# Performance work log

Measured on AMD Instinct MI355X. Metric: run time of the kernel, lower is better.

## Reference

```python
import jax, jax.numpy as jnp
import numpy as np

H = 1024          # h_dim
FF = 4 * H
E = 8             # num_expert
TOP_K = 2


def setup_inputs() -> dict:
    key = jax.random.key(0)
    ks = jax.random.split(key, 7)
    B, S = 4, 2048
    s = 0.02
    return {
        "x": jax.random.normal(ks[0], (B, S, H), dtype=jnp.float32),
        "Wg": jax.random.normal(ks[1], (H, E), dtype=jnp.float32) * s,
        "bg": jnp.zeros((E,), dtype=jnp.float32),
        "W1": jax.random.normal(ks[2], (E, H, FF), dtype=jnp.float32) * s,
        "b1": jnp.zeros((E, FF), dtype=jnp.float32),
        "W2": jax.random.normal(ks[3], (E, FF, H), dtype=jnp.float32) * s,
        "b2": jnp.zeros((E, H), dtype=jnp.float32),
    }


def _moe(x, Wg, bg, W1, b1, W2, b2):
    B, S, h = x.shape
    hs = x.reshape(-1, h)                                  # [T, H]
    logits = hs @ Wg + bg                                  # [T, E]
    probs = jax.nn.softmax(logits.astype(jnp.float32), axis=-1)
    w, idx = jax.lax.top_k(probs, TOP_K)                   # [T, K]
    w = jax.nn.softmax(w, axis=-1).astype(x.dtype)         # renormalize over top-k
    out = jnp.zeros_like(hs)
    for e in range(E):
        # per-token combine weight for expert e (0 if not selected)
        w_e = jnp.sum(w * (idx == e), axis=-1)             # [T]
        y = jax.nn.relu(hs @ W1[e] + b1[e]) @ W2[e] + b2[e]  # [T, H]
        out = out + w_e[:, None] * y
    return out.reshape(B, S, h), logits


def reference(x, Wg, bg, W1, b1, W2, b2):
    return _moe(x, Wg, bg, W1, b1, W2, b2)
```

## Files before the change

kernel.cpp:

```cpp
#include <hip/hip_runtime.h>
#include <hip/hip_bf16.h>

#define T_TOKENS 8192
#define HD 1024
#define FF 4096
#define NEXP 8
#define TOPK 2
#define NR_MAX 17408

typedef __attribute__((ext_vector_type(8))) short bf16x8;
typedef __attribute__((ext_vector_type(4))) float f32x4;

static __device__ __forceinline__ float b2f(ushort u) {
    union { unsigned u; float f; } c; c.u = ((unsigned)u) << 16; return c.f;
}
static __device__ __forceinline__ ushort f2b(float f) {
    union { float f; unsigned u; } c; c.f = f;
    unsigned r = c.u + 0x7fffu + ((c.u >> 16) & 1u);
    return (ushort)(r >> 16);
}

__global__ __launch_bounds__(256) void gate_kernel(
    const float* __restrict__ x, const float* __restrict__ Wg, const float* __restrict__ bg,
    float* __restrict__ logits, int* __restrict__ counts,
    int* __restrict__ e0a, int* __restrict__ e1a,
    float* __restrict__ w0a, float* __restrict__ w1a)
{
    int t = blockIdx.x * 4 + (threadIdx.x >> 6);
    int l = threadIdx.x & 63;
    const float* xr = x + (size_t)t * HD;
    float acc[8] = {0,0,0,0,0,0,0,0};
    #pragma unroll
    for (int i = 0; i < 4; ++i) {
        int h0 = i * 256 + l * 4;
        float4 xv = *(const float4*)(xr + h0);
        #pragma unroll
        for (int j = 0; j < 4; ++j) {
            float xs = (&xv.x)[j];
            const float4* wr = (const float4*)(Wg + (size_t)(h0 + j) * NEXP);
            float4 wa = wr[0], wb = wr[1];
            acc[0] = fmaf(xs, wa.x, acc[0]);
            acc[1] = fmaf(xs, wa.y, acc[1]);
            acc[2] = fmaf(xs, wa.z, acc[2]);
            acc[3] = fmaf(xs, wa.w, acc[3]);
            acc[4] = fmaf(xs, wb.x, acc[4]);
            acc[5] = fmaf(xs, wb.y, acc[5]);
            acc[6] = fmaf(xs, wb.z, acc[6]);
            acc[7] = fmaf(xs, wb.w, acc[7]);
        }
    }
    #pragma unroll
    for (int off = 32; off > 0; off >>= 1) {
        #pragma unroll
        for (int e = 0; e < 8; ++e) acc[e] += __shfl_down(acc[e], off, 64);
    }
    if (l == 0) {
        float lg[8];
        #pragma unroll
        for (int e = 0; e < 8; ++e) {
            lg[e] = acc[e] + bg[e];
            logits[(size_t)t * NEXP + e] = lg[e];
        }
        float m = lg[0];
        #pragma unroll
        for (int e = 1; e < 8; ++e) m = fmaxf(m, lg[e]);
        float p[8], s = 0.f;
        #pragma unroll
        for (int e = 0; e < 8; ++e) { p[e] = expf(lg[e] - m); s += p[e]; }
        float inv = 1.f / s;
        #pragma unroll
        for (int e = 0; e < 8; ++e) p[e] *= inv;
        int i0 = 0;
        #pragma unroll
        for (int e = 1; e < 8; ++e) if (p[e] > p[i0]) i0 = e;
        int i1 = (i0 == 0) ? 1 : 0;
        #pragma unroll
        for (int e = 0; e < 8; ++e) if (e != i0 && p[e] > p[i1]) i1 = e;
        float ed = expf(p[i1] - p[i0]);
        float w0 = 1.f / (1.f + ed);
        float w1 = ed / (1.f + ed);
        e0a[t] = i0; e1a[t] = i1; w0a[t] = w0; w1a[t] = w1;
        atomicAdd(&counts[i0], 1);
        atomicAdd(&counts[i1], 1);
    }
}

__global__ void offsets_kernel(const int* __restrict__ counts, int* __restrict__ off) {
    if (threadIdx.x == 0) {
        int o = 0;
        for (int e = 0; e < 8; ++e) { off[e] = o; o += (counts[e] + 127) & ~127; }
        off[8] = o;
    }
}

__global__ __launch_bounds__(256) void assign_kernel(
    const int* __restrict__ e0a, const int* __restrict__ e1a,
    const int* __restrict__ off, int* __restrict__ fill,
    int* __restrict__ row0, int* __restrict__ row1, int* __restrict__ row_token)
{
    int t = blockIdx.x * 256 + threadIdx.x;
    if (t >= T_TOKENS) return;
    int e0 = e0a[t];
    int r0 = off[e0] + atomicAdd(&fill[e0], 1);
    row0[t] = r0; row_token[r0] = t;
    int e1 = e1a[t];
    int r1 = off[e1] + atomicAdd(&fill[e1], 1);
    row1[t] = r1; row_token[r1] = t;
}

__global__ __launch_bounds__(256) void gather_kernel(
    const float* __restrict__ x, const int* __restrict__ row_token, ushort* __restrict__ Xp)
{
    int r = blockIdx.x;
    int tok = row_token[r];
    int c = threadIdx.x * 4;
    ushort4 o;
    if (tok >= 0 && tok < T_TOKENS) {
        float4 v = *(const float4*)(x + (size_t)tok * HD + c);
        o.x = f2b(v.x); o.y = f2b(v.y); o.z = f2b(v.z); o.w = f2b(v.w);
    } else {
        o.x = 0; o.y = 0; o.z = 0; o.w = 0;
    }
    *(ushort4*)(Xp + (size_t)r * HD + c) = o;
}

__global__ __launch_bounds__(256) void transpose_cvt_kernel(
    const float* __restrict__ in, ushort* __restrict__ out, int R, int C)
{
    __shared__ ushort tile[64][65];
    size_t esz = (size_t)R * C;
    const float* ein = in + (size_t)blockIdx.z * esz;
    ushort* eout = out + (size_t)blockIdx.z * esz;
    int c0 = blockIdx.x * 64, r0 = blockIdx.y * 64;
    int tr = threadIdx.x >> 4;
    int tc = (threadIdx.x & 15) * 4;
    #pragma unroll
    for (int i = 0; i < 4; ++i) {
        int r = tr + i * 16;
        float4 v = *(const float4*)(ein + (size_t)(r0 + r) * C + c0 + tc);
        tile[r][tc + 0] = f2b(v.x);
        tile[r][tc + 1] = f2b(v.y);
        tile[r][tc + 2] = f2b(v.z);
        tile[r][tc + 3] = f2b(v.w);
    }
    __syncthreads();
    #pragma unroll
    for (int i = 0; i < 4; ++i) {
        int cc = tr + i * 16;
        ushort4 o;
        o.x = tile[tc + 0][cc];
        o.y = tile[tc + 1][cc];
        o.z = tile[tc + 2][cc];
        o.w = tile[tc + 3][cc];
        *(ushort4*)(eout + (size_t)(c0 + cc) * R + r0 + tc) = o;
    }
}

template<int K, int NTOT, bool RELU>
__global__ __launch_bounds__(256) void gemm_kernel(
    const ushort* __restrict__ A, const ushort* __restrict__ Bt,
    const float* __restrict__ bias, ushort* __restrict__ Out,
    const int* __restrict__ off)
{
    __shared__ __align__(16) ushort lds[2][2][128 * 32];
    int r0 = blockIdx.y * 128;
    int total = off[8];
    if (r0 >= total) return;
    int e = 0;
    #pragma unroll
    for (int q = 0; q < 7; ++q) if (r0 >= off[q + 1]) e = q + 1;

    int tid = threadIdx.x;
    int w = tid >> 6, lane = tid & 63;
    int wr = w >> 1, wc = w & 1;
    int lr = lane & 15, lk = lane >> 4;
    int ntile = blockIdx.x;

    const ushort* Ab = A + (size_t)r0 * K;
    const ushort* Bb = Bt + (size_t)e * NTOT * K + (size_t)ntile * 128 * K;

    auto stage = [&](const ushort* gbase, ushort* ldsbase) {
        #pragma unroll
        for (int issue = 0; issue < 2; ++issue) {
            int row = issue * 64 + w * 16 + (lane >> 2);
            int chunk = (lane & 3) ^ ((lane >> 3) & 3);
            const ushort* g = gbase + (size_t)row * K + chunk * 8;
            ushort* lp = ldsbase + (issue * 64 + w * 16) * 32;
            __builtin_amdgcn_global_load_lds(
                (const __attribute__((address_space(1))) void*)g,
                (__attribute__((address_space(3))) void*)lp, 16, 0, 0);
        }
    };

    stage(Ab, &lds[0][0][0]);
    stage(Bb, &lds[0][1][0]);

    f32x4 acc[4][4];
    #pragma unroll
    for (int mi = 0; mi < 4; ++mi)
        #pragma unroll
        for (int ni = 0; ni < 4; ++ni) acc[mi][ni] = (f32x4){0.f, 0.f, 0.f, 0.f};

    __syncthreads();

    constexpr int KT = K / 32;
    int cur = 0;
    int slot = lk ^ ((lr >> 1) & 3);
    for (int kt = 0; kt < KT; ++kt) {
        if (kt + 1 < KT) {
            stage(Ab + (kt + 1) * 32, &lds[cur ^ 1][0][0]);
            stage(Bb + (kt + 1) * 32, &lds[cur ^ 1][1][0]);
        }
        const ushort* As = &lds[cur][0][0];
        const ushort* Bs = &lds[cur][1][0];
        bf16x8 a[4], b[4];
        #pragma unroll
        for (int mi = 0; mi < 4; ++mi)
            a[mi] = *(const bf16x8*)(As + (wr * 64 + mi * 16 + lr) * 32 + slot * 8);
        #pragma unroll
        for (int ni = 0; ni < 4; ++ni)
            b[ni] = *(const bf16x8*)(Bs + (wc * 64 + ni * 16 + lr) * 32 + slot * 8);
        #pragma unroll
        for (int mi = 0; mi < 4; ++mi)
            #pragma unroll
            for (int ni = 0; ni < 4; ++ni)
                acc[mi][ni] = __builtin_amdgcn_mfma_f32_16x16x32_bf16(
                    a[mi], b[ni], acc[mi][ni], 0, 0, 0);
        __syncthreads();
        cur ^= 1;
    }

    int c0 = ntile * 128 + wc * 64;
    int rbase = r0 + wr * 64;
    #pragma unroll
    for (int ni = 0; ni < 4; ++ni) {
        int n = c0 + ni * 16 + lr;
        float bv = bias[(size_t)e * NTOT + n];
        #pragma unroll
        for (int mi = 0; mi < 4; ++mi) {
            int m = rbase + mi * 16 + lk * 4;
            #pragma unroll
            for (int j = 0; j < 4; ++j) {
                float v = acc[mi][ni][j] + bv;
                if (RELU) v = fmaxf(v, 0.f);
                Out[(size_t)(m + j) * NTOT + n] = f2b(v);
            }
        }
    }
}

__global__ __launch_bounds__(256) void combine_kernel(
    const ushort* __restrict__ Y, const int* __restrict__ row0, const int* __restrict__ row1,
    const float* __restrict__ w0a, const float* __restrict__ w1a, float* __restrict__ out)
{
    int t = blockIdx.x;
    int c = threadIdx.x * 4;
    int r0 = row0[t], r1 = row1[t];
    float w0 = w0a[t], w1 = w1a[t];
    ushort4 ya = *(const ushort4*)(Y + (size_t)r0 * HD + c);
    ushort4 yb = *(const ushort4*)(Y + (size_t)r1 * HD + c);
    float4 o;
    o.x = w0 * b2f(ya.x) + w1 * b2f(yb.x);
    o.y = w0 * b2f(ya.y) + w1 * b2f(yb.y);
    o.z = w0 * b2f(ya.z) + w1 * b2f(yb.z);
    o.w = w0 * b2f(ya.w) + w1 * b2f(yb.w);
    *(float4*)(out + (size_t)t * HD + c) = o;
}

#define WSA(x) (((x) + 255) & ~(size_t)255)
static constexpr size_t OFF_COUNTS = 0;
static constexpr size_t OFF_FILL   = 64;
static constexpr size_t OFF_OFF    = 128;
static constexpr size_t OFF_E0     = 256;
static constexpr size_t OFF_E1     = OFF_E0 + (size_t)T_TOKENS * 4;
static constexpr size_t OFF_W0     = OFF_E1 + (size_t)T_TOKENS * 4;
static constexpr size_t OFF_W1A    = OFF_W0 + (size_t)T_TOKENS * 4;
static constexpr size_t OFF_R0     = OFF_W1A + (size_t)T_TOKENS * 4;
static constexpr size_t OFF_R1     = OFF_R0 + (size_t)T_TOKENS * 4;
static constexpr size_t OFF_RT     = OFF_R1 + (size_t)T_TOKENS * 4;
static constexpr size_t OFF_XP     = WSA(OFF_RT + (size_t)NR_MAX * 4);
static constexpr size_t OFF_W1T    = OFF_XP  + (size_t)NR_MAX * HD * 2;
static constexpr size_t OFF_W2T    = OFF_W1T + (size_t)NEXP * FF * HD * 2;
static constexpr size_t OFF_H1     = OFF_W2T + (size_t)NEXP * HD * FF * 2;
static constexpr size_t OFF_Y      = OFF_H1  + (size_t)NR_MAX * FF * 2;
static constexpr size_t WS_NEEDED  = OFF_Y   + (size_t)NR_MAX * HD * 2;

extern "C" void kernel_launch(void* const* d_in, const int* in_sizes, int n_in,
                              void* d_out, int out_size, void* d_ws, size_t ws_size,
                              hipStream_t stream) {
    (void)in_sizes; (void)n_in; (void)out_size;
    const float* x  = (const float*)d_in[0];
    const float* Wg = (const float*)d_in[1];
    const float* bg = (const float*)d_in[2];
    const float* W1 = (const float*)d_in[3];
    const float* b1 = (const float*)d_in[4];
    const float* W2 = (const float*)d_in[5];
    const float* b2 = (const float*)d_in[6];
    float* out    = (float*)d_out;
    float* logits = out + (size_t)T_TOKENS * HD;

    if (ws_size < WS_NEEDED) return;

    char* ws = (char*)d_ws;
    int*    counts = (int*)(ws + OFF_COUNTS);
    int*    fill   = (int*)(ws + OFF_FILL);
    int*    offp   = (int*)(ws + OFF_OFF);
    int*    e0a    = (int*)(ws + OFF_E0);
    int*    e1a    = (int*)(ws + OFF_E1);
    float*  w0a    = (float*)(ws + OFF_W0);
    float*  w1a    = (float*)(ws + OFF_W1A);
    int*    row0   = (int*)(ws + OFF_R0);
    int*    row1   = (int*)(ws + OFF_R1);
    int*    rowtok = (int*)(ws + OFF_RT);
    ushort* Xp     = (ushort*)(ws + OFF_XP);
    ushort* W1T    = (ushort*)(ws + OFF_W1T);
    ushort* W2T    = (ushort*)(ws + OFF_W2T);
    ushort* H1     = (ushort*)(ws + OFF_H1);
    ushort* Y      = (ushort*)(ws + OFF_Y);

    hipMemsetAsync(ws, 0, 256, stream);
    hipMemsetAsync(rowtok, 0xFF, (size_t)NR_MAX * 4, stream);

    gate_kernel<<<T_TOKENS / 4, 256, 0, stream>>>(x, Wg, bg, logits, counts, e0a, e1a, w0a, w1a);
    offsets_kernel<<<1, 64, 0, stream>>>(counts, offp);
    assign_kernel<<<T_TOKENS / 256, 256, 0, stream>>>(e0a, e1a, offp, fill, row0, row1, rowtok);
    gather_kernel<<<NR_MAX, 256, 0, stream>>>(x, rowtok, Xp);
    transpose_cvt_kernel<<<dim3(FF / 64, HD / 64, NEXP), 256, 0, stream>>>(W1, W1T, HD, FF);
    transpose_cvt_kernel<<<dim3(HD / 64, FF / 64, NEXP), 256, 0, stream>>>(W2, W2T, FF, HD);
    gemm_kernel<HD, FF, true><<<dim3(FF / 128, NR_MAX / 128), 256, 0, stream>>>(Xp, W1T, b1, H1, offp);
    gemm_kernel<FF, HD, false><<<dim3(HD / 128, NR_MAX / 128), 256, 0, stream>>>(H1, W2T, b2, Y, offp);
    combine_kernel<<<T_TOKENS, 256, 0, stream>>>(Y, row0, row1, w0a, w1a, out);
}
```

Baseline: 794.0 us.

## Rewrite expert GEMMs with 256-row tiles, 8 waves, 4-stage LDS pipeline

```diff
diff --git a/kernel.cpp b/kernel.cpp
--- a/kernel.cpp
+++ b/kernel.cpp
@@ -5,8 +5,7 @@
 #define HD 1024
 #define FF 4096
 #define NEXP 8
-#define TOPK 2
-#define NR_MAX 17408
+#define NR_MAX 18432
 
 typedef __attribute__((ext_vector_type(8))) short bf16x8;
 typedef __attribute__((ext_vector_type(4))) float f32x4;
@@ -88,7 +87,7 @@
 __global__ void offsets_kernel(const int* __restrict__ counts, int* __restrict__ off) {
     if (threadIdx.x == 0) {
         int o = 0;
-        for (int e = 0; e < 8; ++e) { off[e] = o; o += (counts[e] + 127) & ~127; }
+        for (int e = 0; e < 8; ++e) { off[e] = o; o += (counts[e] + 255) & ~255; }
         off[8] = o;
     }
 }
@@ -156,14 +155,32 @@
     }
 }
 
-template<int K, int NTOT, bool RELU>
-__global__ __launch_bounds__(256) void gemm_kernel(
+template<int K, int NTOT, bool RELU, int BN, int WM, int WN>
+__global__ __launch_bounds__(512, 2) void gemm8p_kernel(
     const ushort* __restrict__ A, const ushort* __restrict__ Bt,
     const float* __restrict__ bias, ushort* __restrict__ Out,
     const int* __restrict__ off)
 {
-    __shared__ __align__(16) ushort lds[2][2][128 * 32];
-    int r0 = blockIdx.y * 128;
+    constexpr int BM = 256, BK = 32;
+    constexpr int MREP = BM / (WM * 16);
+    constexpr int NREP = BN / (WN * 16);
+    constexpr int PHASES = (MREP * NREP) / 16;
+    constexpr int MPP = MREP / PHASES;
+    constexpr int A_ISS = (BM * BK) / (512 * 8);
+    constexpr int B_ISS = (BN * BK) / (512 * 8);
+    constexpr int LPT = A_ISS + B_ISS;
+    constexpr int KT = K / BK;
+    constexpr int NT = NTOT / BN;
+
+    __shared__ __align__(16) ushort ldsA[4][BM * BK];
+    __shared__ __align__(16) ushort ldsB[4][BN * BK];
+
+    int nwg = gridDim.x;
+    int bid = blockIdx.x;
+    int wgid = (bid & 7) * (nwg >> 3) + (bid >> 3);
+    int ntile = wgid % NT;
+    int mtile = wgid / NT;
+    int r0 = mtile * BM;
     int total = off[8];
     if (r0 >= total) return;
     int e = 0;
@@ -171,73 +188,122 @@
     for (int q = 0; q < 7; ++q) if (r0 >= off[q + 1]) e = q + 1;
 
     int tid = threadIdx.x;
-    int w = tid >> 6, lane = tid & 63;
-    int wr = w >> 1, wc = w & 1;
+    int wid = tid >> 6, lane = tid & 63;
+    int wr = wid / WN, wc = wid % WN;
     int lr = lane & 15, lk = lane >> 4;
-    int ntile = blockIdx.x;
 
     const ushort* Ab = A + (size_t)r0 * K;
-    const ushort* Bb = Bt + (size_t)e * NTOT * K + (size_t)ntile * 128 * K;
-
-    auto stage = [&](const ushort* gbase, ushort* ldsbase) {
-        #pragma unroll
-        for (int issue = 0; issue < 2; ++issue) {
-            int row = issue * 64 + w * 16 + (lane >> 2);
-            int chunk = (lane & 3) ^ ((lane >> 3) & 3);
-            const ushort* g = gbase + (size_t)row * K + chunk * 8;
-            ushort* lp = ldsbase + (issue * 64 + w * 16) * 32;
+    const ushort* Bb = Bt + ((size_t)e * NTOT + (size_t)ntile * BN) * K;
+
+    int srow = tid >> 2;
+    int schunk = (tid & 3) ^ (srow & 3);
+
+    auto stageA = [&](int kt) {
+        ushort* dst = &ldsA[kt & 3][tid * 8];
+        const ushort* g = Ab + (size_t)kt * BK + (size_t)srow * K + schunk * 8;
+        #pragma unroll
+        for (int i = 0; i < A_ISS; ++i)
             __builtin_amdgcn_global_load_lds(
-                (const __attribute__((address_space(1))) void*)g,
-                (__attribute__((address_space(3))) void*)lp, 16, 0, 0);
+                (const __attribute__((address_space(1))) void*)(g + (size_t)i * 128 * K),
+                (__attribute__((address_space(3))) void*)(dst + i * 4096),
+                16, 0, 0);
+    };
+    auto stageB = [&](int kt) {
+        ushort* dst = &ldsB[kt & 3][tid * 8];
+        const ushort* g = Bb + (size_t)kt * BK + (size_t)srow * K + schunk * 8;
+        #pragma unroll
+        for (int i = 0; i < B_ISS; ++i)
+            __builtin_amdgcn_global_load_lds(
+                (const __attribute__((address_space(1))) void*)(g + (size_t)i * 128 * K),
+                (__attribute__((address_space(3))) void*)(dst + i * 4096),
+                16, 0, 0);
+    };
+    auto ldA = [&](int slot, int m) -> bf16x8 {
+        int row = wr * (BM / WM) + m * 16 + lr;
+        int chunk = lk ^ (row & 3);
+        return *(const bf16x8*)&ldsA[slot][row * 32 + chunk * 8];
+    };
+    auto ldB = [&](int slot, int n) -> bf16x8 {
+        int row = wc * (BN / WN) + n * 16 + lr;
+        int chunk = lk ^ (row & 3);
+        return *(const bf16x8*)&ldsB[slot][row * 32 + chunk * 8];
+    };
+
+    f32x4 acc[MREP][NREP];
+    #pragma unroll
+    for (int m = 0; m < MREP; ++m)
+        #pragma unroll
+        for (int n = 0; n < NREP; ++n) acc[m][n] = (f32x4){0.f, 0.f, 0.f, 0.f};
+
+    stageA(0); stageB(0);
+    stageA(1); stageB(1);
+    stageA(2); stageB(2);
+    asm volatile("s_waitcnt vmcnt(%0)" :: "n"(2 * LPT) : "memory");
+    __builtin_amdgcn_sched_barrier(0);
+    __builtin_amdgcn_s_barrier();
+    __builtin_amdgcn_sched_barrier(0);
+
+    for (int kt = 0; kt < KT; ++kt) {
+        int slot = kt & 3;
+        bf16x8 a0[MPP], b[NREP];
+        #pragma unroll
+        for (int m = 0; m < MPP; ++m) a0[m] = ldA(slot, m);
+        #pragma unroll
+        for (int n = 0; n < NREP; ++n) b[n] = ldB(slot, n);
+        if (kt + 3 < KT) { stageA(kt + 3); if (PHASES == 1) stageB(kt + 3); }
+        __builtin_amdgcn_sched_barrier(0);
+        __builtin_amdgcn_s_barrier();
+        asm volatile("s_waitcnt lgkmcnt(0)" ::: "memory");
+        __builtin_amdgcn_sched_barrier(0);
+        __builtin_amdgcn_s_setprio(1);
+        __builtin_amdgcn_sched_barrier(0);
+        #pragma unroll
+        for (int m = 0; m < MPP; ++m)
+            #pragma unroll
+            for (int n = 0; n < NREP; ++n)
+                acc[m][n] = __builtin_amdgcn_mfma_f32_16x16x32_bf16(a0[m], b[n], acc[m][n], 0, 0, 0);
+        __builtin_amdgcn_sched_barrier(0);
+        __builtin_amdgcn_s_setprio(0);
+        __builtin_amdgcn_sched_barrier(0);
+
+        if constexpr (PHASES == 2) {
+            __builtin_amdgcn_s_barrier();
+            bf16x8 a1[MPP];
+            #pragma unroll
+            for (int m = 0; m < MPP; ++m) a1[m] = ldA(slot, MPP + m);
+            if (kt + 3 < KT) stageB(kt + 3);
+            __builtin_amdgcn_sched_barrier(0);
+            __builtin_amdgcn_s_barrier();
+            asm volatile("s_waitcnt lgkmcnt(0)" ::: "memory");
+            __builtin_amdgcn_sched_barrier(0);
+            __builtin_amdgcn_s_setprio(1);
+            __builtin_amdgcn_sched_barrier(0);
+            #pragma unroll
+            for (int m = 0; m < MPP; ++m)
+                #pragma unroll
+                for (int n = 0; n < NREP; ++n)
+                    acc[MPP + m][n] = __builtin_amdgcn_mfma_f32_16x16x32_bf16(a1[m], b[n], acc[MPP + m][n], 0, 0, 0);
+            __builtin_amdgcn_sched_barrier(0);
+            __builtin_amdgcn_s_setprio(0);
+            __builtin_amdgcn_sched_barrier(0);
         }
-    };
-
-    stage(Ab, &lds[0][0][0]);
-    stage(Bb, &lds[0][1][0]);
-
-    f32x4 acc[4][4];
-    #pragma unroll
-    for (int mi = 0; mi < 4; ++mi)
-        #pragma unroll
-        for (int ni = 0; ni < 4; ++ni) acc[mi][ni] = (f32x4){0.f, 0.f, 0.f, 0.f};
-
-    __syncthreads();
-
-    constexpr int KT = K / 32;
-    int cur = 0;
-    int slot = lk ^ ((lr >> 1) & 3);
-    for (int kt = 0; kt < KT; ++kt) {
-        if (kt + 1 < KT) {
-            stage(Ab + (kt + 1) * 32, &lds[cur ^ 1][0][0]);
-            stage(Bb + (kt + 1) * 32, &lds[cur ^ 1][1][0]);
-        }
-        const ushort* As = &lds[cur][0][0];
-        const ushort* Bs = &lds[cur][1][0];
-        bf16x8 a[4], b[4];
-        #pragma unroll
-        for (int mi = 0; mi < 4; ++mi)
-            a[mi] = *(const bf16x8*)(As + (wr * 64 + mi * 16 + lr) * 32 + slot * 8);
-        #pragma unroll
-        for (int ni = 0; ni < 4; ++ni)
-            b[ni] = *(const bf16x8*)(Bs + (wc * 64 + ni * 16 + lr) * 32 + slot * 8);
-        #pragma unroll
-        for (int mi = 0; mi < 4; ++mi)
-            #pragma unroll
-            for (int ni = 0; ni < 4; ++ni)
-                acc[mi][ni] = __builtin_amdgcn_mfma_f32_16x16x32_bf16(
-                    a[mi], b[ni], acc[mi][ni], 0, 0, 0);
-        __syncthreads();
-        cur ^= 1;
-    }
-
-    int c0 = ntile * 128 + wc * 64;
-    int rbase = r0 + wr * 64;
-    #pragma unroll
-    for (int ni = 0; ni < 4; ++ni) {
+
+        if (kt + 4 <= KT)      { asm volatile("s_waitcnt vmcnt(%0)" :: "n"(2 * LPT) : "memory"); }
+        else if (kt + 3 <= KT) { asm volatile("s_waitcnt vmcnt(%0)" :: "n"(LPT) : "memory"); }
+        else                   { asm volatile("s_waitcnt vmcnt(0)" ::: "memory"); }
+        __builtin_amdgcn_sched_barrier(0);
+        __builtin_amdgcn_s_barrier();
+        __builtin_amdgcn_sched_barrier(0);
+    }
+
+    int c0 = ntile * BN + wc * (BN / WN);
+    int rbase = r0 + wr * (BM / WM);
+    #pragma unroll
+    for (int ni = 0; ni < NREP; ++ni) {
         int n = c0 + ni * 16 + lr;
         float bv = bias[(size_t)e * NTOT + n];
         #pragma unroll
-        for (int mi = 0; mi < 4; ++mi) {
+        for (int mi = 0; mi < MREP; ++mi) {
             int m = rbase + mi * 16 + lk * 4;
             #pragma unroll
             for (int j = 0; j < 4; ++j) {
@@ -327,7 +393,9 @@
     gather_kernel<<<NR_MAX, 256, 0, stream>>>(x, rowtok, Xp);
     transpose_cvt_kernel<<<dim3(FF / 64, HD / 64, NEXP), 256, 0, stream>>>(W1, W1T, HD, FF);
     transpose_cvt_kernel<<<dim3(HD / 64, FF / 64, NEXP), 256, 0, stream>>>(W2, W2T, FF, HD);
-    gemm_kernel<HD, FF, true><<<dim3(FF / 128, NR_MAX / 128), 256, 0, stream>>>(Xp, W1T, b1, H1, offp);
-    gemm_kernel<FF, HD, false><<<dim3(HD / 128, NR_MAX / 128), 256, 0, stream>>>(H1, W2T, b2, Y, offp);
+    gemm8p_kernel<HD, FF, true, 256, 2, 4>
+        <<<(FF / 256) * (NR_MAX / 256), 512, 0, stream>>>(Xp, W1T, b1, H1, offp);
+    gemm8p_kernel<FF, HD, false, 128, 4, 2>
+        <<<(HD / 128) * (NR_MAX / 256), 512, 0, stream>>>(H1, W2T, b2, Y, offp);
     combine_kernel<<<T_TOKENS, 256, 0, stream>>>(Y, row0, row1, w0a, w1a, out);
 }
```

After: 921.0 us. +16.0%, slower.
